# Optimization experiments

Hardware: AMD Instinct MI355X
Metric: run time of the kernel (lower is better)

Reference implementation:

```python
import jax, jax.numpy as jnp
import numpy as np

B, N, DIM = 2, 2048, 1024
HEADS = 16
DIM_HEAD = DIM // HEADS  # 64
SCALE = DIM_HEAD ** -0.5


def setup_inputs() -> dict:
    key = jax.random.key(0)
    k1, k2, k3 = jax.random.split(key, 3)
    x = jax.random.normal(k1, (B, N, DIM), dtype=jnp.float32)
    W_qkv = jax.random.normal(k2, (DIM, 3 * HEADS * DIM_HEAD), dtype=jnp.float32) * (DIM ** -0.5)
    W_out = jax.random.normal(k3, (HEADS * DIM_HEAD, DIM), dtype=jnp.float32) * (DIM ** -0.5)
    return {"x": x, "W_qkv": W_qkv, "W_out": W_out}


def reference(x, W_qkv, W_out):
    b, n, _ = x.shape
    qkv = jnp.einsum('bnd,de->bne', x, W_qkv)  # [b, n, 3*h*dh]
    # faithful to einops 'b n (d k h) -> k b h n d': last axis factored as (dh, 3, h)
    qkv = qkv.reshape(b, n, DIM_HEAD, 3, HEADS)
    qkv = jnp.transpose(qkv, (3, 0, 4, 1, 2))  # [3, b, h, n, dh]
    q, k, v = qkv[0], qkv[1], qkv[2]
    scores = jnp.einsum('bhid,bhjd->bhij', q, k) * SCALE  # [b, h, n, n]
    causal_mask = jnp.triu(jnp.ones((n, n), dtype=bool), k=1)
    scores = jnp.where(causal_mask, -jnp.inf, scores)
    attn = jax.nn.softmax(scores, axis=-1)
    out = jnp.einsum('bhij,bhjd->bhid', attn, v)  # [b, h, n, dh]
    out = jnp.transpose(out, (0, 2, 1, 3)).reshape(b, n, HEADS * DIM_HEAD)  # 'b h n d -> b n (h d)'
    return jnp.einsum('bne,ed->bnd', out, W_out)
```

## Files before the change

kernel.cpp:

```cpp
#include <hip/hip_runtime.h>

typedef _Float16 f16;
typedef f16 half8 __attribute__((ext_vector_type(8)));
typedef f16 f16x4 __attribute__((ext_vector_type(4)));
typedef float f32x4 __attribute__((ext_vector_type(4)));

#define GLOAD_LDS16(gsrc, ldst)                                                              \
  __builtin_amdgcn_global_load_lds((const __attribute__((address_space(1))) void*)(gsrc),    \
                                   (__attribute__((address_space(3))) void*)(ldst), 16, 0, 0)

constexpr float SCALE = 0.125f;
constexpr float SCALE_L2E = 0.125f * 1.4426950408889634f;

static __device__ __forceinline__ unsigned pk2(float a, float b) {
  return __builtin_bit_cast(unsigned, __builtin_amdgcn_cvt_pkrtz(a, b));
}

__global__ __launch_bounds__(256) void k_cvt(const float4* __restrict__ in,
                                             f16x4* __restrict__ out, int n4) {
  int i = blockIdx.x * 256 + threadIdx.x;
  if (i < n4) {
    float4 v = in[i];
    f16x4 o;
    o[0] = (f16)v.x; o[1] = (f16)v.y; o[2] = (f16)v.z; o[3] = (f16)v.w;
    out[i] = o;
  }
}

__global__ __launch_bounds__(256) void k_transpose(const float* __restrict__ in,
                                                   f16* __restrict__ out, int R, int C) {
  __shared__ float t[32][33];
  int c0 = blockIdx.x * 32, r0 = blockIdx.y * 32;
  int tx = threadIdx.x, ty = threadIdx.y;
  for (int i = ty; i < 32; i += 8) t[i][tx] = in[(size_t)(r0 + i) * C + c0 + tx];
  __syncthreads();
  for (int i = ty; i < 32; i += 8) out[(size_t)(c0 + i) * R + r0 + tx] = (f16)t[tx][i];
}

__global__ __launch_bounds__(256) void k_transpose_qkv(const float* __restrict__ in,
                                                       f16* __restrict__ out) {
  __shared__ float t[32][33];
  int c0 = blockIdx.x * 32, r0 = blockIdx.y * 32;
  int tx = threadIdx.x, ty = threadIdx.y;
  for (int i = ty; i < 32; i += 8) t[i][tx] = in[(size_t)(r0 + i) * 3072 + c0 + tx];
  __syncthreads();
  for (int i = ty; i < 32; i += 8) {
    const int e = c0 + i;
    const int d = e / 48, rem = e - d * 48;
    const int k = rem >> 4, h = rem & 15;
    const int ep = k * 1024 + h * 64 + d;
    out[(size_t)ep * 1024 + r0 + tx] = (f16)t[tx][i];
  }
}

template <int MODE>
__global__ __launch_bounds__(256) void k_gemm(const f16* __restrict__ A,
                                              const f16* __restrict__ Bt,
                                              float* __restrict__ C,
                                              f16* __restrict__ Qp,
                                              f16* __restrict__ Kp,
                                              f16* __restrict__ Vt) {
  constexpr int K = 1024, BK = 64;
  __shared__ alignas(16) f16 smem[128 * 128];
  f16* As = smem;
  f16* Bs = smem + 128 * 64;
  const int tid = threadIdx.x;
  const int w = tid >> 6, lane = tid & 63;
  const int g = lane >> 4, lr = lane & 15;
  const int wr = w >> 1, wc = w & 1;
  const int m0 = blockIdx.y * 128, n0 = blockIdx.x * 128;
  const int srow = lane >> 3;
  const int scol = ((lane & 7) ^ srow) << 3;

  f32x4 acc[4][4] = {};

  for (int kt = 0; kt < K; kt += BK) {
    __syncthreads();
#pragma unroll
    for (int i = 0; i < 4; ++i) {
      const int chunk = w * 4 + i;
      const int row = chunk * 8 + srow;
      GLOAD_LDS16(A + (size_t)(m0 + row) * K + kt + scol, &As[chunk * 512]);
      GLOAD_LDS16(Bt + (size_t)(n0 + row) * K + kt + scol, &Bs[chunk * 512]);
    }
    __syncthreads();
#pragma unroll
    for (int c = 0; c < 2; ++c) {
      half8 af[4], bf[4];
#pragma unroll
      for (int m = 0; m < 4; ++m) {
        const int ra = wr * 64 + m * 16 + lr;
        const int off = ra * 128 + ((((c << 2) | g) ^ (ra & 7)) << 4);
        af[m] = *(const half8*)((const char*)As + off);
      }
#pragma unroll
      for (int n = 0; n < 4; ++n) {
        const int rb = wc * 64 + n * 16 + lr;
        const int off = rb * 128 + ((((c << 2) | g) ^ (rb & 7)) << 4);
        bf[n] = *(const half8*)((const char*)Bs + off);
      }
#pragma unroll
      for (int m = 0; m < 4; ++m)
#pragma unroll
        for (int n = 0; n < 4; ++n)
          acc[m][n] = __builtin_amdgcn_mfma_f32_16x16x32_f16(af[m], bf[n], acc[m][n], 0, 0, 0);
    }
  }

  if constexpr (MODE == 0) {
    const int sec = n0 >> 10;
    const int base = n0 & 1023;
    const int b = m0 >> 11;
    if (sec < 2) {
      f16* __restrict__ dst = (sec == 0) ? Qp : Kp;
      const float mul = (sec == 0) ? SCALE_L2E : 1.0f;
#pragma unroll
      for (int n = 0; n < 4; ++n) {
        const int idx = base + wc * 64 + n * 16 + lr;
        const int h = idx >> 6, d = idx & 63;
        f16* __restrict__ dh = dst + ((size_t)(b * 16 + h) * 2048) * 64 + d;
#pragma unroll
        for (int m = 0; m < 4; ++m)
#pragma unroll
          for (int r = 0; r < 4; ++r) {
            const int nn = (m0 & 2047) + wr * 64 + m * 16 + 4 * g + r;
            dh[(size_t)nn * 64] = (f16)(acc[m][n][r] * mul);
          }
      }
    } else {
      char* sb = (char*)smem;
      __syncthreads();
#pragma unroll
      for (int m = 0; m < 4; ++m)
#pragma unroll
        for (int n = 0; n < 4; ++n) {
          const int col = wc * 64 + n * 16 + lr;
          const int tok0 = wr * 64 + m * 16 + 4 * g;
          f16x4 v4;
#pragma unroll
          for (int r = 0; r < 4; ++r) v4[r] = (f16)acc[m][n][r];
          *(f16x4*)(sb + col * 256 + ((tok0 * 2) ^ ((col & 15) << 4))) = v4;
        }
      __syncthreads();
      const int nn0 = m0 & 2047;
#pragma unroll
      for (int pass = 0; pass < 8; ++pass) {
        const int c = w * 32 + pass * 4 + g;
        const int idx = base + c;
        const int h = idx >> 6, d = idx & 63;
        const half8 v = *(const half8*)(sb + c * 256 + ((lr * 16) ^ ((c & 15) << 4)));
        *(half8*)(Vt + ((size_t)(b * 16 + h) * 64 + d) * 2048 + nn0 + lr * 8) = v;
      }
    }
  } else {
#pragma unroll
    for (int m = 0; m < 4; ++m)
#pragma unroll
      for (int n = 0; n < 4; ++n)
#pragma unroll
        for (int r = 0; r < 4; ++r)
          C[(size_t)(m0 + wr * 64 + m * 16 + 4 * g + r) * 1024 +
            (n0 + wc * 64 + n * 16 + lr)] = acc[m][n][r];
  }
}

__global__ __launch_bounds__(128, 3) void k_attn(const f16* __restrict__ Q,
                                                 const f16* __restrict__ Kp,
                                                 const f16* __restrict__ Vt,
                                                 f16* __restrict__ O) {
  __shared__ alignas(16) char plds_all[2][4608];
  const int tid = threadIdx.x;
  const int w = tid >> 6, lane = tid & 63;
  const int g = lane >> 4, lr = lane & 15;
  const int gb = blockIdx.x;
  const int j = 31 - (gb >> 5);
  const int bh = gb & 31;
  const int q0 = (2 * j + w) * 32;
  char* pl = plds_all[w];

  const f16* __restrict__ Qb = Q + (size_t)bh * (2048 * 64);
  const f16* __restrict__ Kb = Kp + (size_t)bh * (2048 * 64);
  const f16* __restrict__ Vb = Vt + (size_t)bh * (64 * 2048);

  half8 qf[2][2];
#pragma unroll
  for (int f = 0; f < 2; ++f)
#pragma unroll
    for (int c = 0; c < 2; ++c)
      qf[f][c] = *(const half8*)(Qb + (size_t)(q0 + 16 * f + lr) * 64 + 32 * c + 8 * g);

  f32x4 acc[2][4] = {};
  float mrow[2] = {-INFINITY, -INFINITY};
  float lrow[2] = {0.f, 0.f};

  for (int kt = 0; kt <= j; ++kt) {
    const int k0 = kt * 64;
    half8 kf[4][2];
#pragma unroll
    for (int jj = 0; jj < 4; ++jj)
#pragma unroll
      for (int c = 0; c < 2; ++c)
        kf[jj][c] = *(const half8*)(Kb + (size_t)(k0 + 16 * jj + lr) * 64 + 32 * c + 8 * g);

    __builtin_amdgcn_s_setprio(1);
    f32x4 st[2][4];
#pragma unroll
    for (int f = 0; f < 2; ++f)
#pragma unroll
      for (int jj = 0; jj < 4; ++jj) {
        f32x4 z = {};
        z = __builtin_amdgcn_mfma_f32_16x16x32_f16(kf[jj][0], qf[f][0], z, 0, 0, 0);
        st[f][jj] = __builtin_amdgcn_mfma_f32_16x16x32_f16(kf[jj][1], qf[f][1], z, 0, 0, 0);
      }
    __builtin_amdgcn_s_setprio(0);

    half8 va[4][2];
#pragma unroll
    for (int nb = 0; nb < 4; ++nb)
#pragma unroll
      for (int c = 0; c < 2; ++c)
        va[nb][c] = *(const half8*)(Vb + (size_t)(16 * nb + lr) * 2048 + k0 + 32 * c + 8 * g);

    if (k0 + 63 > q0) {
#pragma unroll
      for (int f = 0; f < 2; ++f)
#pragma unroll
        for (int jj = 0; jj < 4; ++jj) {
          const int keyb = k0 + 16 * jj + 4 * g;
          const int q = q0 + 16 * f + lr;
#pragma unroll
          for (int r = 0; r < 4; ++r)
            if (keyb + r > q) st[f][jj][r] = -INFINITY;
        }
    }

    float sfv[2];
#pragma unroll
    for (int f = 0; f < 2; ++f) {
      f32x4 m4 = st[f][0];
#pragma unroll
      for (int jj = 1; jj < 4; ++jj)
#pragma unroll
        for (int r = 0; r < 4; ++r) m4[r] = fmaxf(m4[r], st[f][jj][r]);
      float tm = fmaxf(fmaxf(m4[0], m4[1]), fmaxf(m4[2], m4[3]));
      tm = fmaxf(tm, __shfl_xor(tm, 16));
      tm = fmaxf(tm, __shfl_xor(tm, 32));
      const float mn = fmaxf(mrow[f], tm);
      sfv[f] = __builtin_amdgcn_exp2f(mrow[f] - mn);
      mrow[f] = mn;
      f32x4 s4 = {};
#pragma unroll
      for (int jj = 0; jj < 4; ++jj) {
#pragma unroll
        for (int r = 0; r < 4; ++r) {
          st[f][jj][r] = __builtin_amdgcn_exp2f(st[f][jj][r] - mn);
          s4[r] += st[f][jj][r];
        }
        const int rb = (16 * f + lr) * 144 + 32 * jj + 8 * g;
        *(unsigned*)(pl + rb) = pk2(st[f][jj][0], st[f][jj][1]);
        *(unsigned*)(pl + rb + 4) = pk2(st[f][jj][2], st[f][jj][3]);
      }
      float rs = (s4[0] + s4[1]) + (s4[2] + s4[3]);
      rs += __shfl_xor(rs, 16);
      rs += __shfl_xor(rs, 32);
      lrow[f] = lrow[f] * sfv[f] + rs;
#pragma unroll
      for (int nb = 0; nb < 4; ++nb)
#pragma unroll
        for (int r = 0; r < 4; ++r) acc[f][nb][r] *= sfv[f];
    }

    asm volatile("s_waitcnt lgkmcnt(0)" ::: "memory");
    __builtin_amdgcn_sched_barrier(0);
    half8 pf[2][2];
#pragma unroll
    for (int f = 0; f < 2; ++f)
#pragma unroll
      for (int c = 0; c < 2; ++c)
        pf[f][c] = *(const half8*)(pl + (16 * f + lr) * 144 + 64 * c + 16 * g);

    __builtin_amdgcn_s_setprio(1);
#pragma unroll
    for (int f = 0; f < 2; ++f)
#pragma unroll
      for (int nb = 0; nb < 4; ++nb) {
        acc[f][nb] = __builtin_amdgcn_mfma_f32_16x16x32_f16(va[nb][0], pf[f][0], acc[f][nb], 0, 0, 0);
        acc[f][nb] = __builtin_amdgcn_mfma_f32_16x16x32_f16(va[nb][1], pf[f][1], acc[f][nb], 0, 0, 0);
      }
    __builtin_amdgcn_s_setprio(0);
    __builtin_amdgcn_sched_barrier(0);
  }

#pragma unroll
  for (int f = 0; f < 2; ++f) {
    const float inv = 1.f / lrow[f];
#pragma unroll
    for (int nb = 0; nb < 4; ++nb) {
      const int rb = (16 * f + lr) * 144 + 32 * nb + 8 * g;
      *(unsigned*)(pl + rb) = pk2(acc[f][nb][0] * inv, acc[f][nb][1] * inv);
      *(unsigned*)(pl + rb + 4) = pk2(acc[f][nb][2] * inv, acc[f][nb][3] * inv);
    }
  }
  asm volatile("s_waitcnt lgkmcnt(0)" ::: "memory");
  __builtin_amdgcn_sched_barrier(0);
  const int b = bh >> 4, h = bh & 15;
  const int row = lane >> 1, half = lane & 1;
  f16* orow = O + ((size_t)(b * 2048 + q0 + row) * 1024) + h * 64 + 32 * half;
#pragma unroll
  for (int k = 0; k < 4; ++k) {
    const half8 v = *(const half8*)(pl + row * 144 + 64 * half + 16 * k);
    *(half8*)(orow + 8 * k) = v;
  }
}

extern "C" void kernel_launch(void* const* d_in, const int* in_sizes, int n_in,
                              void* d_out, int out_size, void* d_ws, size_t ws_size,
                              hipStream_t stream) {
  const float* x = (const float*)d_in[0];
  const float* Wqkv = (const float*)d_in[1];
  const float* Wout = (const float*)d_in[2];

  char* p = (char*)d_ws;
  f16* Xb = (f16*)p;    p += (size_t)4096 * 1024 * 2;
  f16* Wqkvt = (f16*)p; p += (size_t)3072 * 1024 * 2;
  f16* Woutt = (f16*)p; p += (size_t)1024 * 1024 * 2;
  f16* Qp = (f16*)p;    p += (size_t)32 * 2048 * 64 * 2;
  f16* Kp = (f16*)p;    p += (size_t)32 * 2048 * 64 * 2;
  f16* Vt = (f16*)p;    p += (size_t)32 * 64 * 2048 * 2;
  f16* O = (f16*)p;     p += (size_t)4096 * 1024 * 2;

  k_cvt<<<4096, 256, 0, stream>>>((const float4*)x, (f16x4*)Xb, 4096 * 1024 / 4);
  k_transpose_qkv<<<dim3(96, 32), dim3(32, 8), 0, stream>>>(Wqkv, Wqkvt);
  k_transpose<<<dim3(32, 32), dim3(32, 8), 0, stream>>>(Wout, Woutt, 1024, 1024);
  k_gemm<0><<<dim3(24, 32), 256, 0, stream>>>(Xb, Wqkvt, nullptr, Qp, Kp, Vt);
  k_attn<<<1024, 128, 0, stream>>>(Qp, Kp, Vt, O);
  k_gemm<1><<<dim3(8, 32), 256, 0, stream>>>(O, Woutt, (float*)d_out, nullptr, nullptr, nullptr);
}
```

Before: 229.3 us.

## Split causal attention KV range across blocks and merge partials (flash-decoding style)

```diff
diff --git a/kernel.cpp b/kernel.cpp
--- a/kernel.cpp
+++ b/kernel.cpp
@@ -164,19 +164,30 @@
   }
 }
 
-__global__ __launch_bounds__(128, 3) void k_attn(const f16* __restrict__ Q,
-                                                 const f16* __restrict__ Kp,
-                                                 const f16* __restrict__ Vt,
-                                                 f16* __restrict__ O) {
-  __shared__ alignas(16) char plds_all[2][4608];
-  const int tid = threadIdx.x;
-  const int w = tid >> 6, lane = tid & 63;
+__global__ __launch_bounds__(64, 5) void k_attn(const f16* __restrict__ Q,
+                                                const f16* __restrict__ Kp,
+                                                const f16* __restrict__ Vt,
+                                                f16* __restrict__ O,
+                                                f16* __restrict__ Opart,
+                                                float2* __restrict__ ml) {
+  __shared__ alignas(16) char pl[4608];
+  const int lane = threadIdx.x;
   const int g = lane >> 4, lr = lane & 15;
-  const int gb = blockIdx.x;
-  const int j = 31 - (gb >> 5);
-  const int bh = gb & 31;
-  const int q0 = (2 * j + w) * 32;
-  char* pl = plds_all[w];
+  const int raw = blockIdx.x;
+  const int uid = (raw & 7) * 640 + (raw >> 3);
+  const int bh = uid / 160;
+  const int w = uid - bh * 160;
+  int qt, ks;
+  if (w < 16)       { qt = w;                     ks = 0; }
+  else if (w < 48)  { qt = 16 + ((w - 16) >> 1);  ks = (w - 16) & 1; }
+  else if (w < 96)  { const int v = (w - 48) / 3; qt = 32 + v; ks = (w - 48) - 3 * v; }
+  else              { qt = 48 + ((w - 96) >> 2);  ks = (w - 96) & 3; }
+  const bool single = (w < 16);
+  const int j = qt >> 1;
+  const int kt0 = ks << 3;
+  const int kt1 = min(kt0 + 7, j);
+  const int q0 = qt * 32;
+  const int punit = bh * 144 + (w - 16);
 
   const f16* __restrict__ Qb = Q + (size_t)bh * (2048 * 64);
   const f16* __restrict__ Kb = Kp + (size_t)bh * (2048 * 64);
@@ -193,7 +204,7 @@
   float mrow[2] = {-INFINITY, -INFINITY};
   float lrow[2] = {0.f, 0.f};
 
-  for (int kt = 0; kt <= j; ++kt) {
+  for (int kt = kt0; kt <= kt1; ++kt) {
     const int k0 = kt * 64;
     half8 kf[4][2];
 #pragma unroll
@@ -293,7 +304,7 @@
 
 #pragma unroll
   for (int f = 0; f < 2; ++f) {
-    const float inv = 1.f / lrow[f];
+    const float inv = single ? (1.f / lrow[f]) : 1.f;
 #pragma unroll
     for (int nb = 0; nb < 4; ++nb) {
       const int rb = (16 * f + lr) * 144 + 32 * nb + 8 * g;
@@ -303,13 +314,48 @@
   }
   asm volatile("s_waitcnt lgkmcnt(0)" ::: "memory");
   __builtin_amdgcn_sched_barrier(0);
+  const int row = lane >> 1, half = lane & 1;
+  if (single) {
+    const int b = bh >> 4, h = bh & 15;
+    f16* orow = O + ((size_t)(b * 2048 + q0 + row) * 1024) + h * 64 + 32 * half;
+#pragma unroll
+    for (int k = 0; k < 4; ++k)
+      *(half8*)(orow + 8 * k) = *(const half8*)(pl + row * 144 + 64 * half + 16 * k);
+  } else {
+    if (g == 0) {
+#pragma unroll
+      for (int f = 0; f < 2; ++f)
+        ml[punit * 32 + 16 * f + lr] = make_float2(mrow[f], lrow[f]);
+    }
+    f16* orow = Opart + (size_t)punit * 2048 + row * 64 + 32 * half;
+#pragma unroll
+    for (int k = 0; k < 4; ++k)
+      *(half8*)(orow + 8 * k) = *(const half8*)(pl + row * 144 + 64 * half + 16 * k);
+  }
+}
+
+__global__ __launch_bounds__(64) void k_merge(const f16* __restrict__ Opart,
+                                              const float2* __restrict__ ml,
+                                              f16* __restrict__ O) {
+  const int blk = blockIdx.x;
+  const int bh = blk / 48;
+  const int qt = 16 + (blk - bh * 48);
+  const int nu = (qt < 32) ? 2 : (qt < 48) ? 3 : 4;
+  const int off = (qt < 32) ? (qt - 16) * 2 : (qt < 48) ? 32 + (qt - 32) * 3 : 80 + (qt - 48) * 4;
+  const int pu = bh * 144 + off;
+  const int d = threadIdx.x;
   const int b = bh >> 4, h = bh & 15;
-  const int row = lane >> 1, half = lane & 1;
-  f16* orow = O + ((size_t)(b * 2048 + q0 + row) * 1024) + h * 64 + 32 * half;
-#pragma unroll
-  for (int k = 0; k < 4; ++k) {
-    const half8 v = *(const half8*)(pl + row * 144 + 64 * half + 16 * k);
-    *(half8*)(orow + 8 * k) = v;
+  for (int q = 0; q < 32; ++q) {
+    float mx = -INFINITY;
+    for (int u = 0; u < nu; ++u) mx = fmaxf(mx, ml[(pu + u) * 32 + q].x);
+    float den = 0.f, accum = 0.f;
+    for (int u = 0; u < nu; ++u) {
+      const float2 t = ml[(pu + u) * 32 + q];
+      const float wgt = __builtin_amdgcn_exp2f(t.x - mx);
+      den += wgt * t.y;
+      accum += wgt * (float)Opart[((size_t)(pu + u) * 32 + q) * 64 + d];
+    }
+    O[((size_t)(b * 2048 + qt * 32 + q)) * 1024 + h * 64 + d] = (f16)(accum / den);
   }
 }
 
@@ -321,18 +367,21 @@
   const float* Wout = (const float*)d_in[2];
 
   char* p = (char*)d_ws;
-  f16* Xb = (f16*)p;    p += (size_t)4096 * 1024 * 2;
-  f16* Wqkvt = (f16*)p; p += (size_t)3072 * 1024 * 2;
-  f16* Woutt = (f16*)p; p += (size_t)1024 * 1024 * 2;
-  f16* Qp = (f16*)p;    p += (size_t)32 * 2048 * 64 * 2;
-  f16* Kp = (f16*)p;    p += (size_t)32 * 2048 * 64 * 2;
-  f16* Vt = (f16*)p;    p += (size_t)32 * 64 * 2048 * 2;
-  f16* O = (f16*)p;     p += (size_t)4096 * 1024 * 2;
+  f16* Xb = (f16*)p;      p += (size_t)4096 * 1024 * 2;
+  f16* Wqkvt = (f16*)p;   p += (size_t)3072 * 1024 * 2;
+  f16* Woutt = (f16*)p;   p += (size_t)1024 * 1024 * 2;
+  f16* Qp = (f16*)p;      p += (size_t)32 * 2048 * 64 * 2;
+  f16* Kp = (f16*)p;      p += (size_t)32 * 2048 * 64 * 2;
+  f16* Vt = (f16*)p;      p += (size_t)32 * 64 * 2048 * 2;
+  f16* O = (f16*)p;       p += (size_t)4096 * 1024 * 2;
+  f16* Opart = (f16*)p;   p += (size_t)4608 * 2048 * 2;
+  float2* ml = (float2*)p; p += (size_t)4608 * 32 * 8;
 
   k_cvt<<<4096, 256, 0, stream>>>((const float4*)x, (f16x4*)Xb, 4096 * 1024 / 4);
   k_transpose_qkv<<<dim3(96, 32), dim3(32, 8), 0, stream>>>(Wqkv, Wqkvt);
   k_transpose<<<dim3(32, 32), dim3(32, 8), 0, stream>>>(Wout, Woutt, 1024, 1024);
   k_gemm<0><<<dim3(24, 32), 256, 0, stream>>>(Xb, Wqkvt, nullptr, Qp, Kp, Vt);
-  k_attn<<<1024, 128, 0, stream>>>(Qp, Kp, Vt, O);
+  k_attn<<<5120, 64, 0, stream>>>(Qp, Kp, Vt, O, Opart, ml);
+  k_merge<<<1536, 64, 0, stream>>>(Opart, ml, O);
   k_gemm<1><<<dim3(8, 32), 256, 0, stream>>>(O, Woutt, (float*)d_out, nullptr, nullptr, nullptr);
 }
```

Result: slower. 392.8 us (+71.3%).
